# Kernel tuning notes

Measured on AMD Instinct MI355X. Metric: run time of the kernel, lower is better.

## Reference

```python
import jax, jax.numpy as jnp
import numpy as np

N, IN_C, OUT_C, H = 100000, 256, 64, 8
K_CURV = 1.0      # manifold curvature k (Lorentz: t = sqrt(||s||^2 + k))
POWER_K = 2.0     # power_k of fp feature map


def fp(x, p):
    # norm(x) / (norm(x**p) + eps) * x**p, norms over last dim
    eps = 1e-12
    xp = x ** p
    norm_x = jnp.linalg.norm(x, axis=-1, keepdims=True)
    norm_xp = jnp.linalg.norm(xp, axis=-1, keepdims=True)
    return norm_x / (norm_xp + eps) * xp


def setup_inputs() -> dict:
    key = jax.random.key(0)
    ks = jax.random.split(key, 8)
    s = 1.0 / np.sqrt(IN_C)
    sm = 1.0 / np.sqrt(OUT_C)
    return {
        "query_input": jax.random.normal(ks[0], (N, IN_C), jnp.float32),
        # per-head HypLinear weights (stacked over heads)
        "Wq": jax.random.uniform(ks[1], (H, IN_C, OUT_C), jnp.float32, -s, s),
        "bq": jnp.zeros((H, OUT_C), jnp.float32),
        "Wk": jax.random.uniform(ks[2], (H, IN_C, OUT_C), jnp.float32, -s, s),
        "bk": jnp.zeros((H, OUT_C), jnp.float32),
        "Wv": jax.random.uniform(ks[3], (H, IN_C, OUT_C), jnp.float32, -s, s),
        "bv": jnp.zeros((H, OUT_C), jnp.float32),
        "norm_scale": jnp.ones((), jnp.float32),
        # v_map_mlp: Linear(out_channels, out_channels)
        "Wm": jax.random.uniform(ks[4], (OUT_C, OUT_C), jnp.float32, -sm, sm),
        "bm": jnp.zeros((OUT_C,), jnp.float32),
    }


def reference(query_input, Wq, bq, Wk, bk, Wv, bv, norm_scale, Wm, bm):
    # HypLinear per head: space part = x @ W + b; the time part
    # sqrt(||space||^2 + k) is dropped by [..., 1:] in linear_focus_attention,
    # so only the space components are computed.  shapes: [N, H, OUT_C]
    qs = jnp.einsum('nd,hdo->nho', query_input, Wq) + bq
    ks_ = jnp.einsum('nd,hdo->nho', query_input, Wk) + bk
    v = jnp.einsum('nd,hdo->nho', query_input, Wv) + bv

    denom_s = jnp.abs(norm_scale) + 1e-6
    phi_q = fp((jax.nn.relu(qs) + 1e-6) / denom_s, POWER_K)
    phi_k = fp((jax.nn.relu(ks_) + 1e-6) / denom_s, POWER_K)

    # linear attention: O(N * H * m * d)
    kT_v = jnp.einsum('nhm,nhd->hmd', phi_k, v)          # [H, m, d]
    numerator = jnp.einsum('nhm,hmd->nhd', phi_q, kT_v)  # [N, H, d]
    sum_k = phi_k.sum(axis=0)                            # [H, m]
    denominator = jnp.einsum('nhd,hd->nh', phi_q, sum_k)[..., None]
    attn = numerator / (denominator + 1e-6)

    # residual v-map MLP
    attn = attn + (jnp.einsum('nhd,de->nhe', v, Wm) + bm)

    # trans_heads_concat=False -> mean over heads
    out = attn.mean(axis=1)                              # [N, OUT_C]

    # lift back to Lorentz: prepend time component
    t = jnp.sqrt((out ** 2).sum(axis=-1, keepdims=True) + K_CURV)
    return jnp.concatenate([t, out], axis=-1)            # [N, OUT_C+1]
```

## Files before the change

### kernel.cpp

```cpp
#include <hip/hip_runtime.h>
#include <hip/hip_bf16.h>

#define NROWS 100000
#define NH 8
#define RPC 1568
#define NSUB 49
#define K2CH 98

typedef short s16x8 __attribute__((ext_vector_type(8)));
typedef float f32x4 __attribute__((ext_vector_type(4)));
typedef unsigned short u16;

__device__ __forceinline__ u16 f2bf(float f) {
  union { float f; unsigned u; } x; x.f = f;
  unsigned r = (x.u + 0x7FFFu + ((x.u >> 16) & 1u)) >> 16;
  return (u16)r;
}
__device__ __forceinline__ float bf2f(u16 b) {
  union { unsigned u; float f; } x; x.u = ((unsigned)b) << 16;
  return x.f;
}

__global__ __launch_bounds__(256) void k0_pack(
    const float* __restrict__ Wq, const float* __restrict__ Wk,
    const float* __restrict__ Wv, u16* __restrict__ Wp)
{
  int t = blockIdx.x * 256 + threadIdx.x;
  int lane = t & 63;
  int rest = t >> 6;
  int s = rest % 48;
  int hc = rest / 48;
  int c2 = hc & 1, h = hc >> 1;
  int ml = lane & 15, sgk = lane >> 4;
  const float* W; int col, ks;
  if (s < 32) { int tl = s >> 3; ks = s & 7; W = c2 ? Wk : Wq; col = tl * 16 + ml; }
  else        { int tv = (s >> 3) - 4; ks = s & 7; W = Wv; col = c2 * 32 + tv * 16 + ml; }
  int k0 = ks * 32 + sgk * 8;
  u16 o[8];
#pragma unroll
  for (int j = 0; j < 8; j++)
    o[j] = f2bf(W[((size_t)h * 256 + k0 + j) * 64 + col]);
  ushort4* dst = (ushort4*)(Wp + (size_t)t * 8);
  dst[0] = make_ushort4(o[0], o[1], o[2], o[3]);
  dst[1] = make_ushort4(o[4], o[5], o[6], o[7]);
}

__global__ __launch_bounds__(256, 2) void k1_gemm_phi(
    const float* __restrict__ x, const u16* __restrict__ Wp,
    const float* __restrict__ bq, const float* __restrict__ bk,
    const float* __restrict__ bv, const float* __restrict__ nsc,
    u16* __restrict__ phi_q, u16* __restrict__ phi_k, u16* __restrict__ vout)
{
  __shared__ u16 xs[32 * 256];
  __shared__ u16 vws[32 * 64 * 8];
  __shared__ u16 stq[4 * 16 * 72];
  __shared__ u16 stv[32 * 72];
  __shared__ float biasl[192];

  const int tid = threadIdx.x;
  const int wv = tid >> 6, lane = tid & 63;
  const int c2 = wv & 1, rg = wv >> 1;
  const int m = lane & 15, sg = lane >> 4;
  const int rc = blockIdx.x & 63, h = blockIdx.x >> 6;
  const int n0 = rc * RPC;

  if (tid < 192) {
    const float* bp = tid < 64 ? bq : (tid < 128 ? bk : bv);
    biasl[tid] = bp[h * 64 + (tid & 63)];
  }

  const u16* wb = Wp + (size_t)(h * 2 + c2) * (48 * 64 * 8);
  s16x8 wq[4][8];
#pragma unroll
  for (int t = 0; t < 4; t++)
#pragma unroll
    for (int ks = 0; ks < 8; ks++)
      wq[t][ks] = *(const s16x8*)(wb + ((t * 8 + ks) * 64 + lane) * 8);

#pragma unroll
  for (int i2 = 0; i2 < 8; i2++) {
    int u = tid + i2 * 256;
    int tl = u >> 9, ks = (u >> 6) & 7, ln = u & 63;
    const u16* src = Wp + ((size_t)(h * 2 + (tl >> 1)) * 48 + 32 + (tl & 1) * 8 + ks) * (64 * 8)
                     + (size_t)ln * 8;
    *(s16x8*)(vws + (size_t)u * 8) = *(const s16x8*)src;
  }

#pragma unroll
  for (int i = 0; i < 4; i++) {
    int cu = tid + i * 256;
    int row = cu >> 5, c = cu & 31;
    int n = n0 + row; if (n >= NROWS) n = NROWS - 1;
    const float* src = x + (size_t)n * 256 + c * 8;
    float4 f0 = *(const float4*)src;
    float4 f1 = *(const float4*)(src + 4);
    s16x8 pk;
    pk[0] = (short)f2bf(f0.x); pk[1] = (short)f2bf(f0.y);
    pk[2] = (short)f2bf(f0.z); pk[3] = (short)f2bf(f0.w);
    pk[4] = (short)f2bf(f1.x); pk[5] = (short)f2bf(f1.y);
    pk[6] = (short)f2bf(f1.z); pk[7] = (short)f2bf(f1.w);
    *(s16x8*)(xs + row * 256 + ((c ^ (row & 7)) * 8)) = pk;
  }
  __syncthreads();

  const float inv_denom = 1.0f / (fabsf(nsc[0]) + 1e-6f);
  u16* const xbase = xs + (rg * 16 + m) * 256;
  const int sw = m & 7;

  for (int s = 0; s < NSUB; s++) {
    float4 xl[8];
    if (s + 1 < NSUB) {
      int nb = n0 + (s + 1) * 32;
#pragma unroll
      for (int i = 0; i < 4; i++) {
        int cu = tid + i * 256;
        int row = cu >> 5, c = cu & 31;
        int n = nb + row; if (n >= NROWS) n = NROWS - 1;
        const float* src = x + (size_t)n * 256 + c * 8;
        xl[i * 2]     = *(const float4*)src;
        xl[i * 2 + 1] = *(const float4*)(src + 4);
      }
    }

    f32x4 aq[4], av[2];
#pragma unroll
    for (int t = 0; t < 4; t++) aq[t] = (f32x4){0.f, 0.f, 0.f, 0.f};
    av[0] = (f32x4){0.f, 0.f, 0.f, 0.f};
    av[1] = (f32x4){0.f, 0.f, 0.f, 0.f};
#pragma unroll
    for (int ks = 0; ks < 8; ks++) {
      s16x8 bf = *(const s16x8*)(xbase + (((ks * 4 + sg) ^ sw) * 8));
#pragma unroll
      for (int t = 0; t < 4; t++)
        aq[t] = __builtin_amdgcn_mfma_f32_16x16x32_bf16(wq[t][ks], bf, aq[t], 0, 0, 0);
      s16x8 vw0 = *(const s16x8*)(vws + (((c2 * 2 + 0) * 8 + ks) * 64 + lane) * 8);
      s16x8 vw1 = *(const s16x8*)(vws + (((c2 * 2 + 1) * 8 + ks) * 64 + lane) * 8);
      av[0] = __builtin_amdgcn_mfma_f32_16x16x32_bf16(vw0, bf, av[0], 0, 0, 0);
      av[1] = __builtin_amdgcn_mfma_f32_16x16x32_bf16(vw1, bf, av[1], 0, 0, 0);
    }

    f32x4 bqk[4], bvv[2];
#pragma unroll
    for (int t = 0; t < 4; t++) bqk[t] = *(const f32x4*)&biasl[c2 * 64 + t * 16 + sg * 4];
#pragma unroll
    for (int tv = 0; tv < 2; tv++) bvv[tv] = *(const f32x4*)&biasl[128 + c2 * 32 + tv * 16 + sg * 4];

    float vq[4][4];
    float s2 = 0.f, s4 = 0.f;
#pragma unroll
    for (int t = 0; t < 4; t++)
#pragma unroll
      for (int r = 0; r < 4; r++) {
        float y = (fmaxf(aq[t][r] + bqk[t][r], 0.f) + 1e-6f) * inv_denom;
        float y2 = y * y;
        vq[t][r] = y2;
        s2 += y2; s4 += y2 * y2;
      }
    s2 += __shfl_xor(s2, 16); s2 += __shfl_xor(s2, 32);
    s4 += __shfl_xor(s4, 16); s4 += __shfl_xor(s4, 32);
    float sc = sqrtf(s2) / (sqrtf(s4) + 1e-12f);

    {
      u16* sq = stq + wv * 1152 + m * 72;
#pragma unroll
      for (int t = 0; t < 4; t++)
        *(ushort4*)(sq + ((t + m) & 3) * 16 + sg * 4) =
          make_ushort4(f2bf(vq[t][0] * sc), f2bf(vq[t][1] * sc),
                       f2bf(vq[t][2] * sc), f2bf(vq[t][3] * sc));
      int rowl = rg * 16 + m;
      u16* sv = stv + rowl * 72;
#pragma unroll
      for (int tv = 0; tv < 2; tv++) {
        int tc = c2 * 2 + tv;
        f32x4 a = av[tv], b = bvv[tv];
        *(ushort4*)(sv + ((tc + rowl) & 3) * 16 + sg * 4) =
          make_ushort4(f2bf(a[0] + b[0]), f2bf(a[1] + b[1]),
                       f2bf(a[2] + b[2]), f2bf(a[3] + b[3]));
      }
    }
    {
      int r_ = lane >> 2, tc = lane & 3;
      const u16* a = stq + wv * 1152 + r_ * 72 + ((tc + r_) & 3) * 16;
      s16x8 p0 = *(const s16x8*)a;
      s16x8 p1 = *(const s16x8*)(a + 8);
      int n = n0 + s * 32 + rg * 16 + r_;
      if (n < NROWS) {
        u16* dst = (c2 ? phi_k : phi_q) + ((size_t)h * NROWS + n) * 64 + tc * 16;
        *(s16x8*)dst = p0;
        *(s16x8*)(dst + 8) = p1;
      }
    }
    __syncthreads();

    {
      int row = wv * 8 + (lane >> 3);
      int hc8 = lane & 7, tc = hc8 >> 1, half = hc8 & 1;
      const u16* a = stv + row * 72 + ((tc + row) & 3) * 16 + half * 8;
      s16x8 pv = *(const s16x8*)a;
      int n = n0 + s * 32 + row;
      if (n < NROWS)
        *(s16x8*)(vout + ((size_t)h * NROWS + n) * 64 + tc * 16 + half * 8) = pv;
    }
    if (s + 1 < NSUB) {
#pragma unroll
      for (int i = 0; i < 4; i++) {
        int cu = tid + i * 256;
        int row = cu >> 5, c = cu & 31;
        float4 f0 = xl[i * 2], f1 = xl[i * 2 + 1];
        s16x8 pk;
        pk[0] = (short)f2bf(f0.x); pk[1] = (short)f2bf(f0.y);
        pk[2] = (short)f2bf(f0.z); pk[3] = (short)f2bf(f0.w);
        pk[4] = (short)f2bf(f1.x); pk[5] = (short)f2bf(f1.y);
        pk[6] = (short)f2bf(f1.z); pk[7] = (short)f2bf(f1.w);
        *(s16x8*)(xs + row * 256 + ((c ^ (row & 7)) * 8)) = pk;
      }
    }
    __syncthreads();
  }
}

__global__ __launch_bounds__(256) void k2_ktv(
    const u16* __restrict__ phi_k, const u16* __restrict__ vin,
    float* __restrict__ P)
{
  __shared__ u16 pkT[2][64][72];
  __shared__ u16 vT[2][64][72];
  const int tid = threadIdx.x;
  const int h = blockIdx.y;
  const int r0 = blockIdx.x * 1024;
  const int wv = tid >> 6, lane = tid & 63;
  const int m = lane & 15, sg = lane >> 4;
  const int c4 = (tid & 15) * 4, rgp = tid >> 4;

  const u16* pkb = phi_k + (size_t)h * (NROWS * 64);
  const u16* vb  = vin  + (size_t)h * (NROWS * 64);

  f32x4 acc[4];
#pragma unroll
  for (int t = 0; t < 4; t++) acc[t] = (f32x4){0.f, 0.f, 0.f, 0.f};
  f32x4 accs = (f32x4){0.f, 0.f, 0.f, 0.f};
  s16x8 onesf;
#pragma unroll
  for (int j = 0; j < 8; j++) onesf[j] = (m == 0) ? (short)0x3F80 : (short)0;

  ushort4 pk4[4], vv4[4];
#define K2_LOAD(sub)                                                        \
  {                                                                         \
    int nb = r0 + (sub) * 64 + rgp * 4;                                     \
    _Pragma("unroll")                                                       \
    for (int i = 0; i < 4; i++) {                                           \
      int n = nb + i;                                                       \
      if (n < NROWS) {                                                      \
        pk4[i] = *(const ushort4*)(pkb + (size_t)n * 64 + c4);              \
        vv4[i] = *(const ushort4*)(vb  + (size_t)n * 64 + c4);              \
      } else {                                                              \
        pk4[i] = make_ushort4(0, 0, 0, 0);                                  \
        vv4[i] = make_ushort4(0, 0, 0, 0);                                  \
      }                                                                     \
    }                                                                       \
  }
#define K2_WRITE(buf)                                                       \
  {                                                                         \
    *(ushort4*)&pkT[buf][c4 + 0][rgp * 4] = make_ushort4(pk4[0].x, pk4[1].x, pk4[2].x, pk4[3].x); \
    *(ushort4*)&pkT[buf][c4 + 1][rgp * 4] = make_ushort4(pk4[0].y, pk4[1].y, pk4[2].y, pk4[3].y); \
    *(ushort4*)&pkT[buf][c4 + 2][rgp * 4] = make_ushort4(pk4[0].z, pk4[1].z, pk4[2].z, pk4[3].z); \
    *(ushort4*)&pkT[buf][c4 + 3][rgp * 4] = make_ushort4(pk4[0].w, pk4[1].w, pk4[2].w, pk4[3].w); \
    *(ushort4*)&vT[buf][c4 + 0][rgp * 4]  = make_ushort4(vv4[0].x, vv4[1].x, vv4[2].x, vv4[3].x); \
    *(ushort4*)&vT[buf][c4 + 1][rgp * 4]  = make_ushort4(vv4[0].y, vv4[1].y, vv4[2].y, vv4[3].y); \
    *(ushort4*)&vT[buf][c4 + 2][rgp * 4]  = make_ushort4(vv4[0].z, vv4[1].z, vv4[2].z, vv4[3].z); \
    *(ushort4*)&vT[buf][c4 + 3][rgp * 4]  = make_ushort4(vv4[0].w, vv4[1].w, vv4[2].w, vv4[3].w); \
  }

  K2_LOAD(0); K2_WRITE(0);
  __syncthreads();

  for (int sub = 0; sub < 16; sub++) {
    int cur = sub & 1;
    if (sub + 1 < 16) K2_LOAD(sub + 1);
#pragma unroll
    for (int ks = 0; ks < 2; ks++) {
      s16x8 af = *(const s16x8*)&pkT[cur][wv * 16 + m][ks * 32 + sg * 8];
#pragma unroll
      for (int t = 0; t < 4; t++) {
        s16x8 bfv = *(const s16x8*)&vT[cur][t * 16 + m][ks * 32 + sg * 8];
        acc[t] = __builtin_amdgcn_mfma_f32_16x16x32_bf16(af, bfv, acc[t], 0, 0, 0);
      }
      accs = __builtin_amdgcn_mfma_f32_16x16x32_bf16(af, onesf, accs, 0, 0, 0);
    }
    if (sub + 1 < 16) K2_WRITE(cur ^ 1);
    __syncthreads();
  }

  float* pb = P + (size_t)(blockIdx.x * NH + h) * (65 * 64);
  int mm = wv * 16 + sg * 4;
#pragma unroll
  for (int t = 0; t < 4; t++)
#pragma unroll
    for (int r = 0; r < 4; r++)
      pb[(t * 16 + m) * 64 + mm + r] = acc[t][r];
  if (m == 0)
#pragma unroll
    for (int r = 0; r < 4; r++)
      pb[64 * 64 + mm + r] = accs[r];
}

__global__ __launch_bounds__(256) void k25_pack(
    const float* __restrict__ P, const float* __restrict__ Wm,
    u16* __restrict__ kTvT, u16* __restrict__ WmP)
{
  int idx = blockIdx.x * 256 + threadIdx.x;
  if (idx < NH * 65 * 64) {
    float s = 0.f;
    for (int rcc = 0; rcc < K2CH; rcc++)
      s += P[(size_t)rcc * (NH * 65 * 64) + idx];
    kTvT[idx] = f2bf(s);
  } else if (idx < NH * 65 * 64 + 64 * 64) {
    int j = idx - NH * 65 * 64;
    WmP[j] = f2bf(Wm[(j & 63) * 64 + (j >> 6)]);
  }
}

__global__ __launch_bounds__(256) void k3_out(
    const u16* __restrict__ phi_q, const u16* __restrict__ vin,
    const u16* __restrict__ kTvT, const u16* __restrict__ WmP,
    const float* __restrict__ bm, float* __restrict__ out)
{
  const int tid = threadIdx.x;
  const int wv = tid >> 6, lane = tid & 63;
  const int m = lane & 15, sg = lane >> 4;
  const int n0 = blockIdx.x * 64;
  const int rw = wv * 16;
  const int n = n0 + rw + m;

  float bmv[4];
#pragma unroll
  for (int t = 0; t < 4; t++) bmv[t] = bm[t * 16 + m];

  s16x8 vbf[2];
#pragma unroll
  for (int ks = 0; ks < 2; ks++) {
    float a[8];
#pragma unroll
    for (int j = 0; j < 8; j++) a[j] = 0.f;
#pragma unroll
    for (int h = 0; h < NH; h++) {
      s16x8 v8 = *(const s16x8*)(vin + (size_t)h * (NROWS * 64) + (size_t)n * 64
                                 + ks * 32 + sg * 8);
#pragma unroll
      for (int j = 0; j < 8; j++) a[j] += bf2f((u16)v8[j]);
    }
#pragma unroll
    for (int j = 0; j < 8; j++) vbf[ks][j] = (short)f2bf(a[j] * 0.125f);
  }

  f32x4 zero4 = {0.f, 0.f, 0.f, 0.f};
  s16x8 zero8 = {0, 0, 0, 0, 0, 0, 0, 0};
  f32x4 osum[4];
#pragma unroll
  for (int t = 0; t < 4; t++) osum[t] = zero4;

  for (int h = 0; h < NH; h++) {
    const u16* pqb = phi_q + (size_t)h * (NROWS * 64) + (size_t)n * 64;
    const u16* kb = kTvT + (size_t)h * (65 * 64);
    f32x4 accn[4];
#pragma unroll
    for (int t = 0; t < 4; t++) accn[t] = zero4;
    f32x4 accd = zero4;
#pragma unroll
    for (int ks = 0; ks < 2; ks++) {
      s16x8 aq = *(const s16x8*)(pqb + ks * 32 + sg * 8);
#pragma unroll
      for (int t = 0; t < 4; t++) {
        s16x8 bfv = *(const s16x8*)(kb + (size_t)(t * 16 + m) * 64 + ks * 32 + sg * 8);
        accn[t] = __builtin_amdgcn_mfma_f32_16x16x32_bf16(aq, bfv, accn[t], 0, 0, 0);
      }
      s16x8 bd = zero8;
      if (m == 0)
        bd = *(const s16x8*)(kb + (size_t)64 * 64 + ks * 32 + sg * 8);
      accd = __builtin_amdgcn_mfma_f32_16x16x32_bf16(aq, bd, accd, 0, 0, 0);
    }
#pragma unroll
    for (int r = 0; r < 4; r++) {
      float den = __shfl(accd[r], lane & 48);
      float rinv = 1.0f / (den + 1e-6f);
#pragma unroll
      for (int t = 0; t < 4; t++) osum[t][r] += accn[t][r] * rinv;
    }
  }

  f32x4 accr[4];
#pragma unroll
  for (int t = 0; t < 4; t++) accr[t] = zero4;
#pragma unroll
  for (int ks = 0; ks < 2; ks++)
#pragma unroll
    for (int t = 0; t < 4; t++) {
      s16x8 bw = *(const s16x8*)(WmP + (size_t)(t * 16 + m) * 64 + ks * 32 + sg * 8);
      accr[t] = __builtin_amdgcn_mfma_f32_16x16x32_bf16(vbf[ks], bw, accr[t], 0, 0, 0);
    }

#pragma unroll
  for (int r = 0; r < 4; r++) {
    int nn = n0 + rw + sg * 4 + r;
    float v4[4];
    float ssq = 0.f;
#pragma unroll
    for (int t = 0; t < 4; t++) {
      float o = osum[t][r] * 0.125f + accr[t][r] + bmv[t];
      v4[t] = o;
      ssq += o * o;
    }
    ssq += __shfl_xor(ssq, 1);
    ssq += __shfl_xor(ssq, 2);
    ssq += __shfl_xor(ssq, 4);
    ssq += __shfl_xor(ssq, 8);
    if (nn < NROWS) {
      if (m == 0) out[(size_t)nn * 65] = sqrtf(ssq + 1.0f);
#pragma unroll
      for (int t = 0; t < 4; t++)
        out[(size_t)nn * 65 + 1 + t * 16 + m] = v4[t];
    }
  }
}

extern "C" void kernel_launch(void* const* d_in, const int* in_sizes, int n_in,
                              void* d_out, int out_size, void* d_ws, size_t ws_size,
                              hipStream_t stream) {
  const float* x   = (const float*)d_in[0];
  const float* Wq  = (const float*)d_in[1];
  const float* bq  = (const float*)d_in[2];
  const float* Wk  = (const float*)d_in[3];
  const float* bk  = (const float*)d_in[4];
  const float* Wv  = (const float*)d_in[5];
  const float* bv  = (const float*)d_in[6];
  const float* nsc = (const float*)d_in[7];
  const float* Wm  = (const float*)d_in[8];
  const float* bm  = (const float*)d_in[9];
  float* out = (float*)d_out;

  char* ws = (char*)d_ws;
  const size_t PHI_BYTES = (size_t)NROWS * NH * 64 * 2;
  u16* phi_q = (u16*)(ws);
  u16* phi_k = (u16*)(ws + PHI_BYTES);
  u16* vv    = (u16*)(ws + 2 * PHI_BYTES);
  u16* Wp    = (u16*)(ws + 3 * PHI_BYTES);
  char* p    = ws + 3 * PHI_BYTES + 786432;
  float* P   = (float*)(p);
  u16* kTvT  = (u16*)(p + 13066240);
  u16* WmP   = (u16*)(p + 13066240 + 66560);

  k0_pack<<<192, 256, 0, stream>>>(Wq, Wk, Wv, Wp);
  k1_gemm_phi<<<512, 256, 0, stream>>>(x, Wp, bq, bk, bv, nsc, phi_q, phi_k, vv);
  dim3 g2(K2CH, NH);
  k2_ktv<<<g2, 256, 0, stream>>>(phi_k, vv, P);
  k25_pack<<<(NH * 65 * 64 + 64 * 64 + 255) / 256, 256, 0, stream>>>(P, Wm, kTvT, WmP);
  k3_out<<<(NROWS + 63) / 64, 256, 0, stream>>>(phi_q, vv, kTvT, WmP, bm, out);
}
```

Measured before the change: 449.1 us.

## Fuse phi_k^T·v reduction into projection GEMM kernel, drop phi_k buffer

```diff
diff --git a/kernel.cpp b/kernel.cpp
--- a/kernel.cpp
+++ b/kernel.cpp
@@ -5,7 +5,7 @@
 #define NH 8
 #define RPC 1568
 #define NSUB 49
-#define K2CH 98
+#define NCH1 64
 
 typedef short s16x8 __attribute__((ext_vector_type(8)));
 typedef float f32x4 __attribute__((ext_vector_type(4)));
@@ -49,12 +49,14 @@
     const float* __restrict__ x, const u16* __restrict__ Wp,
     const float* __restrict__ bq, const float* __restrict__ bk,
     const float* __restrict__ bv, const float* __restrict__ nsc,
-    u16* __restrict__ phi_q, u16* __restrict__ phi_k, u16* __restrict__ vout)
+    u16* __restrict__ phi_q, u16* __restrict__ vout, float* __restrict__ P)
 {
   __shared__ u16 xs[32 * 256];
   __shared__ u16 vws[32 * 64 * 8];
   __shared__ u16 stq[4 * 16 * 72];
   __shared__ u16 stv[32 * 72];
+  __shared__ u16 tks[64 * 40];
+  __shared__ u16 tvs[64 * 40];
   __shared__ float biasl[192];
 
   const int tid = threadIdx.x;
@@ -107,6 +109,14 @@
   u16* const xbase = xs + (rg * 16 + m) * 256;
   const int sw = m & 7;
 
+  f32x4 kacc[4];
+#pragma unroll
+  for (int t = 0; t < 4; t++) kacc[t] = (f32x4){0.f, 0.f, 0.f, 0.f};
+  f32x4 ksum = (f32x4){0.f, 0.f, 0.f, 0.f};
+  s16x8 onesf;
+#pragma unroll
+  for (int j = 0; j < 8; j++) onesf[j] = (m == 0) ? (short)0x3F80 : (short)0;
+
   for (int s = 0; s < NSUB; s++) {
     float4 xl[8];
     if (s + 1 < NSUB) {
@@ -161,31 +171,44 @@
     float sc = sqrtf(s2) / (sqrtf(s4) + 1e-12f);
 
     {
-      u16* sq = stq + wv * 1152 + m * 72;
-#pragma unroll
-      for (int t = 0; t < 4; t++)
-        *(ushort4*)(sq + ((t + m) & 3) * 16 + sg * 4) =
-          make_ushort4(f2bf(vq[t][0] * sc), f2bf(vq[t][1] * sc),
-                       f2bf(vq[t][2] * sc), f2bf(vq[t][3] * sc));
       int rowl = rg * 16 + m;
+      if (!c2) {
+        u16* sq = stq + wv * 1152 + m * 72;
+#pragma unroll
+        for (int t = 0; t < 4; t++)
+          *(ushort4*)(sq + ((t + m) & 3) * 16 + sg * 4) =
+            make_ushort4(f2bf(vq[t][0] * sc), f2bf(vq[t][1] * sc),
+                         f2bf(vq[t][2] * sc), f2bf(vq[t][3] * sc));
+      } else {
+#pragma unroll
+        for (int t = 0; t < 4; t++)
+#pragma unroll
+          for (int r = 0; r < 4; r++)
+            tks[(t * 16 + sg * 4 + r) * 40 + rowl] = f2bf(vq[t][r] * sc);
+      }
       u16* sv = stv + rowl * 72;
 #pragma unroll
       for (int tv = 0; tv < 2; tv++) {
         int tc = c2 * 2 + tv;
         f32x4 a = av[tv], b = bvv[tv];
-        *(ushort4*)(sv + ((tc + rowl) & 3) * 16 + sg * 4) =
-          make_ushort4(f2bf(a[0] + b[0]), f2bf(a[1] + b[1]),
-                       f2bf(a[2] + b[2]), f2bf(a[3] + b[3]));
-      }
-    }
-    {
+        u16 e0 = f2bf(a[0] + b[0]), e1 = f2bf(a[1] + b[1]);
+        u16 e2 = f2bf(a[2] + b[2]), e3 = f2bf(a[3] + b[3]);
+        *(ushort4*)(sv + ((tc + rowl) & 3) * 16 + sg * 4) = make_ushort4(e0, e1, e2, e3);
+        int chb = (tc * 16 + sg * 4) * 40 + rowl;
+        tvs[chb]       = e0;
+        tvs[chb + 40]  = e1;
+        tvs[chb + 80]  = e2;
+        tvs[chb + 120] = e3;
+      }
+    }
+    if (!c2) {
       int r_ = lane >> 2, tc = lane & 3;
       const u16* a = stq + wv * 1152 + r_ * 72 + ((tc + r_) & 3) * 16;
       s16x8 p0 = *(const s16x8*)a;
       s16x8 p1 = *(const s16x8*)(a + 8);
       int n = n0 + s * 32 + rg * 16 + r_;
       if (n < NROWS) {
-        u16* dst = (c2 ? phi_k : phi_q) + ((size_t)h * NROWS + n) * 64 + tc * 16;
+        u16* dst = phi_q + ((size_t)h * NROWS + n) * 64 + tc * 16;
         *(s16x8*)dst = p0;
         *(s16x8*)(dst + 8) = p1;
       }
@@ -201,6 +224,17 @@
       if (n < NROWS)
         *(s16x8*)(vout + ((size_t)h * NROWS + n) * 64 + tc * 16 + half * 8) = pv;
     }
+
+    if (n0 + s * 32 < NROWS) {
+      s16x8 af = *(const s16x8*)(tks + (wv * 16 + m) * 40 + sg * 8);
+#pragma unroll
+      for (int dcb = 0; dcb < 4; dcb++) {
+        s16x8 bfv = *(const s16x8*)(tvs + (dcb * 16 + m) * 40 + sg * 8);
+        kacc[dcb] = __builtin_amdgcn_mfma_f32_16x16x32_bf16(af, bfv, kacc[dcb], 0, 0, 0);
+      }
+      ksum = __builtin_amdgcn_mfma_f32_16x16x32_bf16(af, onesf, ksum, 0, 0, 0);
+    }
+
     if (s + 1 < NSUB) {
 #pragma unroll
       for (int i = 0; i < 4; i++) {
@@ -217,91 +251,20 @@
     }
     __syncthreads();
   }
-}
-
-__global__ __launch_bounds__(256) void k2_ktv(
-    const u16* __restrict__ phi_k, const u16* __restrict__ vin,
-    float* __restrict__ P)
-{
-  __shared__ u16 pkT[2][64][72];
-  __shared__ u16 vT[2][64][72];
-  const int tid = threadIdx.x;
-  const int h = blockIdx.y;
-  const int r0 = blockIdx.x * 1024;
-  const int wv = tid >> 6, lane = tid & 63;
-  const int m = lane & 15, sg = lane >> 4;
-  const int c4 = (tid & 15) * 4, rgp = tid >> 4;
-
-  const u16* pkb = phi_k + (size_t)h * (NROWS * 64);
-  const u16* vb  = vin  + (size_t)h * (NROWS * 64);
-
-  f32x4 acc[4];
-#pragma unroll
-  for (int t = 0; t < 4; t++) acc[t] = (f32x4){0.f, 0.f, 0.f, 0.f};
-  f32x4 accs = (f32x4){0.f, 0.f, 0.f, 0.f};
-  s16x8 onesf;
-#pragma unroll
-  for (int j = 0; j < 8; j++) onesf[j] = (m == 0) ? (short)0x3F80 : (short)0;
-
-  ushort4 pk4[4], vv4[4];
-#define K2_LOAD(sub)                                                        \
-  {                                                                         \
-    int nb = r0 + (sub) * 64 + rgp * 4;                                     \
-    _Pragma("unroll")                                                       \
-    for (int i = 0; i < 4; i++) {                                           \
-      int n = nb + i;                                                       \
-      if (n < NROWS) {                                                      \
-        pk4[i] = *(const ushort4*)(pkb + (size_t)n * 64 + c4);              \
-        vv4[i] = *(const ushort4*)(vb  + (size_t)n * 64 + c4);              \
-      } else {                                                              \
-        pk4[i] = make_ushort4(0, 0, 0, 0);                                  \
-        vv4[i] = make_ushort4(0, 0, 0, 0);                                  \
-      }                                                                     \
-    }                                                                       \
-  }
-#define K2_WRITE(buf)                                                       \
-  {                                                                         \
-    *(ushort4*)&pkT[buf][c4 + 0][rgp * 4] = make_ushort4(pk4[0].x, pk4[1].x, pk4[2].x, pk4[3].x); \
-    *(ushort4*)&pkT[buf][c4 + 1][rgp * 4] = make_ushort4(pk4[0].y, pk4[1].y, pk4[2].y, pk4[3].y); \
-    *(ushort4*)&pkT[buf][c4 + 2][rgp * 4] = make_ushort4(pk4[0].z, pk4[1].z, pk4[2].z, pk4[3].z); \
-    *(ushort4*)&pkT[buf][c4 + 3][rgp * 4] = make_ushort4(pk4[0].w, pk4[1].w, pk4[2].w, pk4[3].w); \
-    *(ushort4*)&vT[buf][c4 + 0][rgp * 4]  = make_ushort4(vv4[0].x, vv4[1].x, vv4[2].x, vv4[3].x); \
-    *(ushort4*)&vT[buf][c4 + 1][rgp * 4]  = make_ushort4(vv4[0].y, vv4[1].y, vv4[2].y, vv4[3].y); \
-    *(ushort4*)&vT[buf][c4 + 2][rgp * 4]  = make_ushort4(vv4[0].z, vv4[1].z, vv4[2].z, vv4[3].z); \
-    *(ushort4*)&vT[buf][c4 + 3][rgp * 4]  = make_ushort4(vv4[0].w, vv4[1].w, vv4[2].w, vv4[3].w); \
-  }
-
-  K2_LOAD(0); K2_WRITE(0);
-  __syncthreads();
-
-  for (int sub = 0; sub < 16; sub++) {
-    int cur = sub & 1;
-    if (sub + 1 < 16) K2_LOAD(sub + 1);
-#pragma unroll
-    for (int ks = 0; ks < 2; ks++) {
-      s16x8 af = *(const s16x8*)&pkT[cur][wv * 16 + m][ks * 32 + sg * 8];
-#pragma unroll
-      for (int t = 0; t < 4; t++) {
-        s16x8 bfv = *(const s16x8*)&vT[cur][t * 16 + m][ks * 32 + sg * 8];
-        acc[t] = __builtin_amdgcn_mfma_f32_16x16x32_bf16(af, bfv, acc[t], 0, 0, 0);
-      }
-      accs = __builtin_amdgcn_mfma_f32_16x16x32_bf16(af, onesf, accs, 0, 0, 0);
-    }
-    if (sub + 1 < 16) K2_WRITE(cur ^ 1);
-    __syncthreads();
-  }
-
-  float* pb = P + (size_t)(blockIdx.x * NH + h) * (65 * 64);
-  int mm = wv * 16 + sg * 4;
-#pragma unroll
-  for (int t = 0; t < 4; t++)
-#pragma unroll
-    for (int r = 0; r < 4; r++)
-      pb[(t * 16 + m) * 64 + mm + r] = acc[t][r];
-  if (m == 0)
-#pragma unroll
-    for (int r = 0; r < 4; r++)
-      pb[64 * 64 + mm + r] = accs[r];
+
+  {
+    float* pb = P + (size_t)(rc * NH + h) * (65 * 64);
+    int mm = wv * 16 + sg * 4;
+#pragma unroll
+    for (int dcb = 0; dcb < 4; dcb++)
+#pragma unroll
+      for (int r = 0; r < 4; r++)
+        pb[(dcb * 16 + m) * 64 + mm + r] = kacc[dcb][r];
+    if (m == 0)
+#pragma unroll
+      for (int r = 0; r < 4; r++)
+        pb[64 * 64 + mm + r] = ksum[r];
+  }
 }
 
 __global__ __launch_bounds__(256) void k25_pack(
@@ -311,7 +274,7 @@
   int idx = blockIdx.x * 256 + threadIdx.x;
   if (idx < NH * 65 * 64) {
     float s = 0.f;
-    for (int rcc = 0; rcc < K2CH; rcc++)
+    for (int rcc = 0; rcc < NCH1; rcc++)
       s += P[(size_t)rcc * (NH * 65 * 64) + idx];
     kTvT[idx] = f2bf(s);
   } else if (idx < NH * 65 * 64 + 64 * 64) {
@@ -441,18 +404,15 @@
   char* ws = (char*)d_ws;
   const size_t PHI_BYTES = (size_t)NROWS * NH * 64 * 2;
   u16* phi_q = (u16*)(ws);
-  u16* phi_k = (u16*)(ws + PHI_BYTES);
-  u16* vv    = (u16*)(ws + 2 * PHI_BYTES);
-  u16* Wp    = (u16*)(ws + 3 * PHI_BYTES);
-  char* p    = ws + 3 * PHI_BYTES + 786432;
+  u16* vv    = (u16*)(ws + PHI_BYTES);
+  u16* Wp    = (u16*)(ws + 2 * PHI_BYTES);
+  char* p    = ws + 2 * PHI_BYTES + 786432;
   float* P   = (float*)(p);
-  u16* kTvT  = (u16*)(p + 13066240);
-  u16* WmP   = (u16*)(p + 13066240 + 66560);
+  u16* kTvT  = (u16*)(p + 8519680);
+  u16* WmP   = (u16*)(p + 8519680 + 66560);
 
   k0_pack<<<192, 256, 0, stream>>>(Wq, Wk, Wv, Wp);
-  k1_gemm_phi<<<512, 256, 0, stream>>>(x, Wp, bq, bk, bv, nsc, phi_q, phi_k, vv);
-  dim3 g2(K2CH, NH);
-  k2_ktv<<<g2, 256, 0, stream>>>(phi_k, vv, P);
+  k1_gemm_phi<<<512, 256, 0, stream>>>(x, Wp, bq, bk, bv, nsc, phi_q, vv, P);
   k25_pack<<<(NH * 65 * 64 + 64 * 64 + 255) / 256, 256, 0, stream>>>(P, Wm, kTvT, WmP);
   k3_out<<<(NROWS + 63) / 64, 256, 0, stream>>>(phi_q, vv, kTvT, WmP, bm, out);
 }
```

New measurement: 490.2 us. 1.09x slower.

## Stage kTv and Wm in swizzled LDS, prefetch phi_q, fuse v-mean into head loop

Applied to the files above, without the earlier changes.

```diff
diff --git a/kernel.cpp b/kernel.cpp
--- a/kernel.cpp
+++ b/kernel.cpp
@@ -320,38 +320,30 @@
   }
 }
 
-__global__ __launch_bounds__(256) void k3_out(
+__global__ __launch_bounds__(512, 4) void k3_out(
     const u16* __restrict__ phi_q, const u16* __restrict__ vin,
     const u16* __restrict__ kTvT, const u16* __restrict__ WmP,
     const float* __restrict__ bm, float* __restrict__ out)
 {
+  __shared__ u16 kbl[37376];
+
   const int tid = threadIdx.x;
   const int wv = tid >> 6, lane = tid & 63;
   const int m = lane & 15, sg = lane >> 4;
-  const int n0 = blockIdx.x * 64;
+  const int n0 = blockIdx.x * 128;
   const int rw = wv * 16;
   const int n = n0 + rw + m;
 
-  float bmv[4];
-#pragma unroll
-  for (int t = 0; t < 4; t++) bmv[t] = bm[t * 16 + m];
-
-  s16x8 vbf[2];
-#pragma unroll
-  for (int ks = 0; ks < 2; ks++) {
-    float a[8];
-#pragma unroll
-    for (int j = 0; j < 8; j++) a[j] = 0.f;
-#pragma unroll
-    for (int h = 0; h < NH; h++) {
-      s16x8 v8 = *(const s16x8*)(vin + (size_t)h * (NROWS * 64) + (size_t)n * 64
-                                 + ks * 32 + sg * 8);
-#pragma unroll
-      for (int j = 0; j < 8; j++) a[j] += bf2f((u16)v8[j]);
-    }
-#pragma unroll
-    for (int j = 0; j < 8; j++) vbf[ks][j] = (short)f2bf(a[j] * 0.125f);
-  }
+  for (int i = tid; i < 4672; i += 512) {
+    int e0 = i * 8;
+    s16x8 val = *(const s16x8*)(kTvT + e0);
+    int r = e0 >> 6;
+    *(s16x8*)&kbl[e0 ^ ((r & 7) << 3)] = val;
+  }
+  __syncthreads();
+
+#define KBL_FRAG(rowlin, off) \
+  (*(const s16x8*)&kbl[(((rowlin) * 64 + (off)) ^ (((rowlin) & 7) << 3))])
 
   f32x4 zero4 = {0.f, 0.f, 0.f, 0.f};
   s16x8 zero8 = {0, 0, 0, 0, 0, 0, 0, 0};
@@ -359,26 +351,58 @@
 #pragma unroll
   for (int t = 0; t < 4; t++) osum[t] = zero4;
 
+  float va[2][8];
+#pragma unroll
+  for (int ks = 0; ks < 2; ks++)
+#pragma unroll
+    for (int j = 0; j < 8; j++) va[ks][j] = 0.f;
+
+  s16x8 aqn[2];
+#pragma unroll
+  for (int ks = 0; ks < 2; ks++)
+    aqn[ks] = *(const s16x8*)(phi_q + (size_t)n * 64 + ks * 32 + sg * 8);
+
   for (int h = 0; h < NH; h++) {
-    const u16* pqb = phi_q + (size_t)h * (NROWS * 64) + (size_t)n * 64;
-    const u16* kb = kTvT + (size_t)h * (65 * 64);
+    s16x8 aq0 = aqn[0], aq1 = aqn[1];
+    s16x8 v80 = *(const s16x8*)(vin + (size_t)h * (NROWS * 64) + (size_t)n * 64 + sg * 8);
+    s16x8 v81 = *(const s16x8*)(vin + (size_t)h * (NROWS * 64) + (size_t)n * 64 + 32 + sg * 8);
+    if (h + 1 < NH) {
+      const u16* pq = phi_q + (size_t)(h + 1) * (NROWS * 64) + (size_t)n * 64;
+      aqn[0] = *(const s16x8*)(pq + sg * 8);
+      aqn[1] = *(const s16x8*)(pq + 32 + sg * 8);
+    }
+
+    const int rl = h * 65;
     f32x4 accn[4];
 #pragma unroll
     for (int t = 0; t < 4; t++) accn[t] = zero4;
     f32x4 accd = zero4;
-#pragma unroll
-    for (int ks = 0; ks < 2; ks++) {
-      s16x8 aq = *(const s16x8*)(pqb + ks * 32 + sg * 8);
+    {
 #pragma unroll
       for (int t = 0; t < 4; t++) {
-        s16x8 bfv = *(const s16x8*)(kb + (size_t)(t * 16 + m) * 64 + ks * 32 + sg * 8);
-        accn[t] = __builtin_amdgcn_mfma_f32_16x16x32_bf16(aq, bfv, accn[t], 0, 0, 0);
+        s16x8 bfv = KBL_FRAG(rl + t * 16 + m, sg * 8);
+        accn[t] = __builtin_amdgcn_mfma_f32_16x16x32_bf16(aq0, bfv, accn[t], 0, 0, 0);
       }
       s16x8 bd = zero8;
-      if (m == 0)
-        bd = *(const s16x8*)(kb + (size_t)64 * 64 + ks * 32 + sg * 8);
-      accd = __builtin_amdgcn_mfma_f32_16x16x32_bf16(aq, bd, accd, 0, 0, 0);
-    }
+      if (m == 0) bd = KBL_FRAG(rl + 64, sg * 8);
+      accd = __builtin_amdgcn_mfma_f32_16x16x32_bf16(aq0, bd, accd, 0, 0, 0);
+    }
+    {
+#pragma unroll
+      for (int t = 0; t < 4; t++) {
+        s16x8 bfv = KBL_FRAG(rl + t * 16 + m, 32 + sg * 8);
+        accn[t] = __builtin_amdgcn_mfma_f32_16x16x32_bf16(aq1, bfv, accn[t], 0, 0, 0);
+      }
+      s16x8 bd = zero8;
+      if (m == 0) bd = KBL_FRAG(rl + 64, 32 + sg * 8);
+      accd = __builtin_amdgcn_mfma_f32_16x16x32_bf16(aq1, bd, accd, 0, 0, 0);
+    }
+
+#pragma unroll
+    for (int j = 0; j < 8; j++) va[0][j] += bf2f((u16)v80[j]);
+#pragma unroll
+    for (int j = 0; j < 8; j++) va[1][j] += bf2f((u16)v81[j]);
+
 #pragma unroll
     for (int r = 0; r < 4; r++) {
       float den = __shfl(accd[r], lane & 48);
@@ -388,6 +412,12 @@
     }
   }
 
+  s16x8 vbf[2];
+#pragma unroll
+  for (int ks = 0; ks < 2; ks++)
+#pragma unroll
+    for (int j = 0; j < 8; j++) vbf[ks][j] = (short)f2bf(va[ks][j] * 0.125f);
+
   f32x4 accr[4];
 #pragma unroll
   for (int t = 0; t < 4; t++) accr[t] = zero4;
@@ -395,9 +425,13 @@
   for (int ks = 0; ks < 2; ks++)
 #pragma unroll
     for (int t = 0; t < 4; t++) {
-      s16x8 bw = *(const s16x8*)(WmP + (size_t)(t * 16 + m) * 64 + ks * 32 + sg * 8);
+      s16x8 bw = KBL_FRAG(520 + t * 16 + m, ks * 32 + sg * 8);
       accr[t] = __builtin_amdgcn_mfma_f32_16x16x32_bf16(vbf[ks], bw, accr[t], 0, 0, 0);
     }
+
+  float bmv[4];
+#pragma unroll
+  for (int t = 0; t < 4; t++) bmv[t] = bm[t * 16 + m];
 
 #pragma unroll
   for (int r = 0; r < 4; r++) {
@@ -454,5 +488,5 @@
   dim3 g2(K2CH, NH);
   k2_ktv<<<g2, 256, 0, stream>>>(phi_k, vv, P);
   k25_pack<<<(NH * 65 * 64 + 64 * 64 + 255) / 256, 256, 0, stream>>>(P, Wm, kTvT, WmP);
-  k3_out<<<(NROWS + 63) / 64, 256, 0, stream>>>(phi_q, vv, kTvT, WmP, bm, out);
-}
+  k3_out<<<(NROWS + 127) / 128, 512, 0, stream>>>(phi_q, vv, kTvT, WmP, bm, out);
+}
```

Result: slower. 492.5 us (+9.6%).
